# Kernel tuning notes

Hardware: AMD Instinct MI355X
Metric: run time of the kernel (lower is better)

Reference implementation:

```python
import jax, jax.numpy as jnp
import numpy as np

W = 1e6
HUBER = 0.005
N0 = 5  # timesteps dropped at window start


def _skew(v):
    x, y, z = v[..., 0], v[..., 1], v[..., 2]
    o = jnp.zeros_like(x)
    return jnp.stack([
        jnp.stack([o, -z, y], -1),
        jnp.stack([z, o, -x], -1),
        jnp.stack([-y, x, o], -1)], -2)


def so3_exp(phi):
    """Rodrigues formula: rotation vector (...,3) -> rotation matrix (...,3,3)."""
    t2 = jnp.sum(phi * phi, axis=-1)[..., None, None]  # theta^2, (...,1,1)
    small = t2 < 1e-8
    safe_t2 = jnp.where(small, 1.0, t2)
    theta = jnp.sqrt(safe_t2)
    A = jnp.where(small, 1.0 - t2 / 6.0, jnp.sin(theta) / theta)
    B = jnp.where(small, 0.5 - t2 / 24.0, (1.0 - jnp.cos(theta)) / safe_t2)
    K = _skew(phi)
    I = jnp.eye(3, dtype=phi.dtype)
    return I + A * K + B * (K @ K)


def so3_log(R):
    """Rotation matrix (...,3,3) -> rotation vector (...,3)."""
    tr = R[..., 0, 0] + R[..., 1, 1] + R[..., 2, 2]
    cos = jnp.clip(0.5 * (tr - 1.0), -1.0, 1.0)
    small = cos > 1.0 - 1e-6
    safe_cos = jnp.where(small, 0.0, cos)
    angle = jnp.arccos(safe_cos)
    factor = jnp.where(small, 0.5, angle / (2.0 * jnp.sin(angle)))
    vee = jnp.stack([
        R[..., 2, 1] - R[..., 1, 2],
        R[..., 0, 2] - R[..., 2, 0],
        R[..., 1, 0] - R[..., 0, 1]], -1)
    return factor[..., None] * vee


def _bmtm(a, b):
    # batched a^T @ b
    return jnp.einsum('nji,njk->nik', a, b)


def setup_inputs() -> dict:
    key = jax.random.key(0)
    k1, k2 = jax.random.split(key)
    N, T = 64, 8192
    xs = 0.3 * jax.random.normal(k1, (N, T, 9), dtype=jnp.float32)
    hat_xs = 0.3 * jax.random.normal(k2, (N, T, 15), dtype=jnp.float32)
    return {"xs": xs, "hat_xs": hat_xs}


def reference(xs, hat_xs):
    N = xs.shape[0]
    x = xs.reshape(-1, 9)
    omegas_xs, dv_xs, dp_xs = x[:, :3], x[:, 3:6], x[:, 6:9]
    Omegas_Xs = so3_exp(omegas_xs)

    h = hat_xs.reshape(-1, 15)
    hat_Omegas = so3_exp(h[:, :3])
    hat_acc = h[:, 3:6]
    hat_Xi = so3_exp(h[:, 6:9])
    hat_dv = h[:, 9:12]
    hat_dp = h[:, 12:15]

    rs1 = 6.0 * so3_log(_bmtm(Omegas_Xs, hat_Omegas)).reshape(N, -1, 3)[:, N0:]
    rs2 = 6.0 * (dv_xs - hat_acc).reshape(N, -1, 3)[:, N0:]
    rs3 = so3_log(_bmtm(Omegas_Xs, hat_Xi)).reshape(N, -1, 3)[:, N0:]
    rs4 = (dv_xs - hat_dv).reshape(N, -1, 3)[:, N0:]
    rs5 = (dp_xs - hat_dp).reshape(N, -1, 3)[:, N0:]
    rs = jnp.concatenate((rs1, rs2, rs3, rs4, rs5), axis=2)

    # SmoothL1Loss(beta=1, reduction='mean') on rs/huber vs zeros
    z = rs / HUBER
    az = jnp.abs(z)
    sl = jnp.mean(jnp.where(az < 1.0, 0.5 * z * z, az - 0.5))
    return W * sl * (HUBER ** 2)
```

## Files before the change

### kernel.cpp

```cpp
#include <hip/hip_runtime.h>
#include <math.h>


namespace {
constexpr int kN = 64;
constexpr int kT = 8192;
constexpr int kN0 = 5;
constexpr int kRows = kN * kT;
constexpr int kRowsPerBlock = 256;
constexpr int kBlocks = kRows / kRowsPerBlock;
constexpr int kWavesPerBlock = kRowsPerBlock / 64;
constexpr int kPartials = kBlocks * kWavesPerBlock;
constexpr int kXs4 = kRowsPerBlock * 9 / 4;
constexpr int kHx4 = kRowsPerBlock * 15 / 4;
constexpr float kScale = (float)(25.0 / ((double)kN * (double)(kT - kN0) * 15.0));
}

__device__ __forceinline__ float fast_acos(float x) {
    float xa = fabsf(x);
    float p = fmaf(xa, fmaf(xa, fmaf(xa, -0.0187293f, 0.0742610f), -0.2121144f), 1.5707288f);
    float r = sqrtf(fmaxf(1.0f - xa, 0.0f)) * p;
    return x < 0.0f ? 3.14159265f - r : r;
}

__device__ __forceinline__ void so3_exp9(float x, float y, float z, float R[9]) {
    float t2 = x * x + y * y + z * z;
    bool sm = t2 < 1e-8f;
    float st2 = sm ? 1.0f : t2;
    float rth = rsqrtf(st2);
    float th = st2 * rth;
    float s, c;
    __sincosf(th, &s, &c);
    float A = sm ? (1.0f - t2 * (1.0f / 6.0f)) : (s * rth);
    float B = sm ? (0.5f - t2 * (1.0f / 24.0f)) : ((1.0f - c) * rth * rth);
    R[0] = 1.0f - B * (y * y + z * z);
    R[1] = B * x * y - A * z;
    R[2] = B * x * z + A * y;
    R[3] = B * x * y + A * z;
    R[4] = 1.0f - B * (x * x + z * z);
    R[5] = B * y * z - A * x;
    R[6] = B * x * z - A * y;
    R[7] = B * y * z + A * x;
    R[8] = 1.0f - B * (x * x + y * y);
}

__device__ __forceinline__ void bmtm_log(const float a[9], const float b[9], float out[3]) {
    float C00 = a[0] * b[0] + a[3] * b[3] + a[6] * b[6];
    float C11 = a[1] * b[1] + a[4] * b[4] + a[7] * b[7];
    float C22 = a[2] * b[2] + a[5] * b[5] + a[8] * b[8];
    float C21 = a[2] * b[1] + a[5] * b[4] + a[8] * b[7];
    float C12 = a[1] * b[2] + a[4] * b[5] + a[7] * b[8];
    float C02 = a[0] * b[2] + a[3] * b[5] + a[6] * b[8];
    float C20 = a[2] * b[0] + a[5] * b[3] + a[8] * b[6];
    float C10 = a[1] * b[0] + a[4] * b[3] + a[7] * b[6];
    float C01 = a[0] * b[1] + a[3] * b[4] + a[6] * b[7];
    float tr = C00 + C11 + C22;
    float cs = 0.5f * (tr - 1.0f);
    cs = fminf(1.0f, fmaxf(-1.0f, cs));
    bool sm = cs > (1.0f - 1e-6f);
    float ang = fast_acos(sm ? 0.0f : cs);
    float factor = sm ? 0.5f : 0.5f * ang * rsqrtf(fmaxf(1.0f - cs * cs, 1e-30f));
    out[0] = factor * (C21 - C12);
    out[1] = factor * (C02 - C20);
    out[2] = factor * (C10 - C01);
}

__device__ __forceinline__ float huber_term(float r) {
    float z = r * 200.0f;
    float az = fabsf(z);
    return az < 1.0f ? 0.5f * z * z : az - 0.5f;
}

__global__ __launch_bounds__(256) void gyro_loss_kernel(
    const float* __restrict__ xs, const float* __restrict__ hx,
    float* __restrict__ partials) {
    __shared__ __align__(16) float s_xs[kRowsPerBlock * 9];
    __shared__ __align__(16) float s_hx[kRowsPerBlock * 15];
    const int tid = threadIdx.x;
    const long base_row = (long)blockIdx.x * kRowsPerBlock;

    const float4* gx4 = reinterpret_cast<const float4*>(xs + base_row * 9);
    const float4* gh4 = reinterpret_cast<const float4*>(hx + base_row * 15);
    float4* sx4 = reinterpret_cast<float4*>(s_xs);
    float4* sh4 = reinterpret_cast<float4*>(s_hx);
#pragma unroll
    for (int i = tid; i < kXs4; i += kRowsPerBlock) sx4[i] = gx4[i];
#pragma unroll
    for (int i = tid; i < kHx4; i += kRowsPerBlock) sh4[i] = gh4[i];
    __syncthreads();

    const int row = (int)base_row + tid;
    const int t = row & (kT - 1);
    float sum = 0.0f;
    if (t >= kN0) {
        const float* x = s_xs + tid * 9;
        const float* h = s_hx + tid * 15;
        float Rw[9], Ro[9], Rx[9];
        so3_exp9(x[0], x[1], x[2], Rw);
        so3_exp9(h[0], h[1], h[2], Ro);
        so3_exp9(h[6], h[7], h[8], Rx);
        float l1[3], l3[3];
        bmtm_log(Rw, Ro, l1);
        bmtm_log(Rw, Rx, l3);
        sum += huber_term(6.0f * l1[0]) + huber_term(6.0f * l1[1]) + huber_term(6.0f * l1[2]);
        sum += huber_term(6.0f * (x[3] - h[3])) + huber_term(6.0f * (x[4] - h[4])) +
               huber_term(6.0f * (x[5] - h[5]));
        sum += huber_term(l3[0]) + huber_term(l3[1]) + huber_term(l3[2]);
        sum += huber_term(x[3] - h[9]) + huber_term(x[4] - h[10]) + huber_term(x[5] - h[11]);
        sum += huber_term(x[6] - h[12]) + huber_term(x[7] - h[13]) + huber_term(x[8] - h[14]);
    }

#pragma unroll
    for (int off = 32; off > 0; off >>= 1) sum += __shfl_down(sum, off, 64);
    if ((tid & 63) == 0) partials[blockIdx.x * kWavesPerBlock + (tid >> 6)] = sum;
}

__global__ __launch_bounds__(256) void reduce_kernel(const float* __restrict__ partials,
                                                     float* __restrict__ out) {
    const int tid = threadIdx.x;
    const float4* p4 = reinterpret_cast<const float4*>(partials);
    float sum = 0.0f;
#pragma unroll
    for (int i = 0; i < kPartials / 4 / 256; ++i) {
        float4 v = p4[tid + i * 256];
        sum += (v.x + v.y) + (v.z + v.w);
    }
#pragma unroll
    for (int off = 32; off > 0; off >>= 1) sum += __shfl_down(sum, off, 64);
    __shared__ float wsum[4];
    if ((tid & 63) == 0) wsum[tid >> 6] = sum;
    __syncthreads();
    if (tid == 0) out[0] = (wsum[0] + wsum[1] + wsum[2] + wsum[3]) * kScale;
}

extern "C" void kernel_launch(void* const* d_in, const int* in_sizes, int n_in,
                              void* d_out, int out_size, void* d_ws, size_t ws_size,
                              hipStream_t stream) {
    const float* xs = (const float*)d_in[0];
    const float* hx = (const float*)d_in[1];
    float* out = (float*)d_out;
    float* partials = (float*)d_ws;
    gyro_loss_kernel<<<kBlocks, kRowsPerBlock, 0, stream>>>(xs, hx, partials);
    reduce_kernel<<<1, 256, 0, stream>>>(partials, out);
}
```

Measured before the change: 88.47 us.

## Process four rows per thread with direct vector loads, dropping LDS staging

Each thread now loads four consecutive rows straight into registers with float4 loads and computes them in an unrolled loop, replacing the shared-memory staging and block barrier. This is meant to remove LDS traffic and the sync, and to add instruction-level parallelism. In exchange, register pressure rises, the grid shrinks to a quarter as many blocks, and per-thread global accesses become strided, which may reduce occupancy and latency hiding.

After: 90.72 us. 1.03x slower.

```diff
diff --git a/kernel.cpp b/kernel.cpp
--- a/kernel.cpp
+++ b/kernel.cpp
@@ -7,12 +7,12 @@
 constexpr int kT = 8192;
 constexpr int kN0 = 5;
 constexpr int kRows = kN * kT;
-constexpr int kRowsPerBlock = 256;
+constexpr int kRowsPerThread = 4;
+constexpr int kThreadsPerBlock = 256;
+constexpr int kRowsPerBlock = kThreadsPerBlock * kRowsPerThread;
 constexpr int kBlocks = kRows / kRowsPerBlock;
-constexpr int kWavesPerBlock = kRowsPerBlock / 64;
+constexpr int kWavesPerBlock = kThreadsPerBlock / 64;
 constexpr int kPartials = kBlocks * kWavesPerBlock;
-constexpr int kXs4 = kRowsPerBlock * 9 / 4;
-constexpr int kHx4 = kRowsPerBlock * 15 / 4;
 constexpr float kScale = (float)(25.0 / ((double)kN * (double)(kT - kN0) * 15.0));
 }
 
@@ -74,40 +74,44 @@
 __global__ __launch_bounds__(256) void gyro_loss_kernel(
     const float* __restrict__ xs, const float* __restrict__ hx,
     float* __restrict__ partials) {
-    __shared__ __align__(16) float s_xs[kRowsPerBlock * 9];
-    __shared__ __align__(16) float s_hx[kRowsPerBlock * 15];
     const int tid = threadIdx.x;
-    const long base_row = (long)blockIdx.x * kRowsPerBlock;
+    const long chunk = (long)blockIdx.x * kThreadsPerBlock + tid;
+    const long row0 = chunk * kRowsPerThread;
 
-    const float4* gx4 = reinterpret_cast<const float4*>(xs + base_row * 9);
-    const float4* gh4 = reinterpret_cast<const float4*>(hx + base_row * 15);
-    float4* sx4 = reinterpret_cast<float4*>(s_xs);
-    float4* sh4 = reinterpret_cast<float4*>(s_hx);
+    const float4* xp = reinterpret_cast<const float4*>(xs + row0 * 9);
+    const float4* hp = reinterpret_cast<const float4*>(hx + row0 * 15);
+    float a[36], h[60];
 #pragma unroll
-    for (int i = tid; i < kXs4; i += kRowsPerBlock) sx4[i] = gx4[i];
+    for (int i = 0; i < 9; ++i) {
+        float4 v = xp[i];
+        a[4 * i] = v.x; a[4 * i + 1] = v.y; a[4 * i + 2] = v.z; a[4 * i + 3] = v.w;
+    }
 #pragma unroll
-    for (int i = tid; i < kHx4; i += kRowsPerBlock) sh4[i] = gh4[i];
-    __syncthreads();
+    for (int i = 0; i < 15; ++i) {
+        float4 v = hp[i];
+        h[4 * i] = v.x; h[4 * i + 1] = v.y; h[4 * i + 2] = v.z; h[4 * i + 3] = v.w;
+    }
 
-    const int row = (int)base_row + tid;
-    const int t = row & (kT - 1);
     float sum = 0.0f;
-    if (t >= kN0) {
-        const float* x = s_xs + tid * 9;
-        const float* h = s_hx + tid * 15;
+    const int t0 = (int)(row0 & (kT - 1));
+#pragma unroll
+    for (int j = 0; j < kRowsPerThread; ++j) {
+        if (t0 + j < kN0) continue;
+        const float* x = a + 9 * j;
+        const float* hh = h + 15 * j;
         float Rw[9], Ro[9], Rx[9];
         so3_exp9(x[0], x[1], x[2], Rw);
-        so3_exp9(h[0], h[1], h[2], Ro);
-        so3_exp9(h[6], h[7], h[8], Rx);
+        so3_exp9(hh[0], hh[1], hh[2], Ro);
+        so3_exp9(hh[6], hh[7], hh[8], Rx);
         float l1[3], l3[3];
         bmtm_log(Rw, Ro, l1);
         bmtm_log(Rw, Rx, l3);
         sum += huber_term(6.0f * l1[0]) + huber_term(6.0f * l1[1]) + huber_term(6.0f * l1[2]);
-        sum += huber_term(6.0f * (x[3] - h[3])) + huber_term(6.0f * (x[4] - h[4])) +
-               huber_term(6.0f * (x[5] - h[5]));
+        sum += huber_term(6.0f * (x[3] - hh[3])) + huber_term(6.0f * (x[4] - hh[4])) +
+               huber_term(6.0f * (x[5] - hh[5]));
         sum += huber_term(l3[0]) + huber_term(l3[1]) + huber_term(l3[2]);
-        sum += huber_term(x[3] - h[9]) + huber_term(x[4] - h[10]) + huber_term(x[5] - h[11]);
-        sum += huber_term(x[6] - h[12]) + huber_term(x[7] - h[13]) + huber_term(x[8] - h[14]);
+        sum += huber_term(x[3] - hh[9]) + huber_term(x[4] - hh[10]) + huber_term(x[5] - hh[11]);
+        sum += huber_term(x[6] - hh[12]) + huber_term(x[7] - hh[13]) + huber_term(x[8] - hh[14]);
     }
 
 #pragma unroll
@@ -140,6 +144,6 @@
     const float* hx = (const float*)d_in[1];
     float* out = (float*)d_out;
     float* partials = (float*)d_ws;
-    gyro_loss_kernel<<<kBlocks, kRowsPerBlock, 0, stream>>>(xs, hx, partials);
+    gyro_loss_kernel<<<kBlocks, kThreadsPerBlock, 0, stream>>>(xs, hx, partials);
     reduce_kernel<<<1, 256, 0, stream>>>(partials, out);
 }
```
